# Kernel optimization log

Hardware: AMD Instinct MI355X
Metric: run time of the kernel (lower is better)

The kernel has to match this reference:

```python
import jax, jax.numpy as jnp
import numpy as np

N_NODES = 50000
N_EDGES = 1600000
F_IN = 512      # 2 * embedding_dimension
HID = 512
OUT = 4
NEG_SLOPE = 0.01  # torch LeakyReLU default


def _leaky_relu(x):
    return jnp.where(x >= 0, x, NEG_SLOPE * x)


def setup_inputs() -> dict:
    key = jax.random.key(0)
    ks = jax.random.split(key, 12)
    s_in = 1.0 / np.sqrt(F_IN)
    s_h = 1.0 / np.sqrt(HID)
    return {
        "feature": jax.random.normal(ks[0], (N_NODES, F_IN), jnp.float32),
        "edge_index": jax.random.randint(ks[1], (2, N_EDGES), 0, N_NODES, jnp.int64),
        "edge_type": jax.random.randint(ks[2], (N_EDGES,), 0, 2, jnp.int64),
        # input MLP
        "W_in": jax.random.uniform(ks[3], (F_IN, HID), jnp.float32, -s_in, s_in),
        "b_in": jnp.zeros((HID,), jnp.float32),
        # sage1: lin_l (bias) on aggregated neighbors, lin_r (no bias) on self
        "W1_l": jax.random.uniform(ks[4], (HID, HID), jnp.float32, -s_h, s_h),
        "b1_l": jnp.zeros((HID,), jnp.float32),
        "W1_r": jax.random.uniform(ks[5], (HID, HID), jnp.float32, -s_h, s_h),
        # sage2
        "W2_l": jax.random.uniform(ks[6], (HID, HID), jnp.float32, -s_h, s_h),
        "b2_l": jnp.zeros((HID,), jnp.float32),
        "W2_r": jax.random.uniform(ks[7], (HID, HID), jnp.float32, -s_h, s_h),
        # output linear (hidden -> 4); note forward skips linear_relu_output1
        "W_out": jax.random.uniform(ks[8], (HID, OUT), jnp.float32, -s_h, s_h),
        "b_out": jnp.zeros((OUT,), jnp.float32),
    }


def _sage_conv(x, src, dst, W_l, b_l, W_r):
    # mean aggregation of source features onto destinations (PyG default flow)
    agg = jax.ops.segment_sum(x[src], dst, num_segments=N_NODES)  # [N, H]
    cnt = jax.ops.segment_sum(jnp.ones((src.shape[0], 1), x.dtype), dst,
                              num_segments=N_NODES)               # [N, 1]
    mean = agg / jnp.maximum(cnt, 1.0)
    return mean @ W_l + b_l + x @ W_r


def reference(feature, edge_index, edge_type,
              W_in, b_in, W1_l, b1_l, W1_r, W2_l, b2_l, W2_r, W_out, b_out):
    src, dst = edge_index[0], edge_index[1]
    x = _leaky_relu(feature.astype(jnp.float32) @ W_in + b_in)
    x = _sage_conv(x, src, dst, W1_l, b1_l, W1_r)
    # dropout is identity in eval mode
    x = _sage_conv(x, src, dst, W2_l, b2_l, W2_r)
    return x @ W_out + b_out
```

## Files before the change

kernel.cpp:

```cpp
#include <hip/hip_runtime.h>
#include <stdint.h>

#define NNODES 50000
#define NEDGES 1600000
#define HID 512
#define NEG_SLOPE 0.01f
#define NBUCK 98
#define NBLK 200
#define TILE 8000
#define NSUB 8
#define GPBLK 391
#define MROWS 50048
#define NNB 8

#define TCBLK 1024
#define CABLK 12512
#define SABLK 1025
#define PREP_CA (TCBLK)
#define PREP_SA (TCBLK + CABLK)
#define PREP_HK (TCBLK + CABLK + SABLK)
#define PREP_GRID (PREP_HK + NBLK)

typedef __attribute__((ext_vector_type(8))) short bf16x8;
typedef __attribute__((ext_vector_type(8))) unsigned short u16x8;
typedef __attribute__((ext_vector_type(4))) float f32x4;

__device__ __forceinline__ unsigned short f2bf(float f) {
  unsigned int u = __builtin_bit_cast(unsigned int, f);
  u += 0x7FFFu + ((u >> 16) & 1u);
  return (unsigned short)(u >> 16);
}
__device__ __forceinline__ void gload_lds16(const void* g, void* l) {
  __builtin_amdgcn_global_load_lds(
      (const __attribute__((address_space(1))) void*)g,
      (__attribute__((address_space(3))) void*)l, 16, 0, 0);
}

__device__ __forceinline__ float wave_dot(const float* __restrict__ Arow,
                                          const float* __restrict__ B, int j) {
  int l = threadIdx.x & 63;
  float4 a0 = *reinterpret_cast<const float4*>(Arow + l * 8);
  float4 a1 = *reinterpret_cast<const float4*>(Arow + l * 8 + 4);
  const float* bb = B + (size_t)(l * 8) * 4 + j;
  float s = a0.x * bb[0] + a0.y * bb[4] + a0.z * bb[8] + a0.w * bb[12] +
            a1.x * bb[16] + a1.y * bb[20] + a1.z * bb[24] + a1.w * bb[28];
#pragma unroll
  for (int off = 1; off < 64; off <<= 1) s += __shfl_xor(s, off);
  return s;
}

__global__ __launch_bounds__(256) void prep(
    const float* __restrict__ feat, const float* __restrict__ W_in,
    const float* __restrict__ W2l, const float* __restrict__ W2r,
    const float* __restrict__ Wout, const float* __restrict__ b2l,
    const float* __restrict__ bout, const int* __restrict__ ei,
    unsigned short* __restrict__ Wt0, unsigned short* __restrict__ featb,
    float* __restrict__ Wlp, float* __restrict__ Wrp, float* __restrict__ bp,
    int* __restrict__ hist) {
  __shared__ int h[NBUCK];
  __shared__ int flg;
  int blk = blockIdx.x, t = threadIdx.x;
  if (blk < PREP_CA) {
    int i = blk * 256 + t;
    int n = i >> 9, k = i & 511;
    Wt0[i] = f2bf(W_in[(k << 9) | n]);
  } else if (blk < PREP_SA) {
    int idx = (blk - PREP_CA) * 256 + t;
    size_t g = (size_t)idx * 8;
    int row = idx >> 6;
    u16x8 pk;
    if (row < NNODES) {
      float4 v0 = *reinterpret_cast<const float4*>(feat + g);
      float4 v1 = *reinterpret_cast<const float4*>(feat + g + 4);
      pk[0] = f2bf(v0.x); pk[1] = f2bf(v0.y); pk[2] = f2bf(v0.z); pk[3] = f2bf(v0.w);
      pk[4] = f2bf(v1.x); pk[5] = f2bf(v1.y); pk[6] = f2bf(v1.z); pk[7] = f2bf(v1.w);
    } else {
      pk = (u16x8)0;
    }
    *reinterpret_cast<u16x8*>(featb + g) = pk;
  } else if (blk < PREP_HK) {
    int gw = (blk - PREP_SA) * 4 + (t >> 6);
    int l = t & 63;
    if (gw < 2048) {
      float v = wave_dot(W2l + (size_t)(gw >> 2) * 512, Wout, gw & 3);
      if (l == 0) Wlp[gw] = v;
    } else if (gw < 4096) {
      int g = gw - 2048;
      float v = wave_dot(W2r + (size_t)(g >> 2) * 512, Wout, g & 3);
      if (l == 0) Wrp[g] = v;
    } else if (gw < 4100) {
      int j = gw - 4096;
      float v = wave_dot(b2l, Wout, j);
      if (l == 0) bp[j] = v + bout[j];
    }
  } else {
    int hb = blk - PREP_HK;
    for (int i = t; i < NBUCK; i += 256) h[i] = 0;
    if (t < 64) {
      unsigned long long m = __ballot(ei[2 * t + 1] != 0);
      if (t == 0) flg = (m != 0ULL) ? 1 : 0;
    }
    __syncthreads();
    int f = flg;
    int e0 = hb * TILE;
    for (int e = e0 + 2 * t; e < e0 + TILE; e += 512) {
      int d0, d1;
      if (f) {
        int2 v = *reinterpret_cast<const int2*>(&ei[(size_t)NEDGES + e]);
        d0 = v.x; d1 = v.y;
      } else {
        int4 v = *reinterpret_cast<const int4*>(&ei[2 * ((size_t)NEDGES + e)]);
        d0 = v.x; d1 = v.z;
      }
      if ((unsigned)d0 < NNODES) atomicAdd(&h[d0 >> 9], 1);
      if ((unsigned)d1 < NNODES) atomicAdd(&h[d1 >> 9], 1);
    }
    __syncthreads();
    for (int i = t; i < NBUCK; i += 256) hist[i * NBLK + hb] = h[i];
  }
}

__global__ __launch_bounds__(256) void smallB(
    const float* __restrict__ W1l, const float* __restrict__ W1r,
    const float* __restrict__ b1l,
    const float* __restrict__ Wlp, const float* __restrict__ Wrp,
    const float* __restrict__ bp,
    float* __restrict__ Pall, float* __restrict__ kb, float* __restrict__ kc) {
  int gw = blockIdx.x * 4 + (threadIdx.x >> 6);
  int l = threadIdx.x & 63;
  if (gw < 6144) {
    int k = gw / 12, jg = gw % 12;
    int g = jg >> 2, j = jg & 3;
    float v;
    if (g == 0) v = wave_dot(W1l + (size_t)k * 512, Wlp, j);
    else if (g == 1) v = wave_dot(W1r + (size_t)k * 512, Wlp, j) +
                         wave_dot(W1l + (size_t)k * 512, Wrp, j);
    else v = wave_dot(W1r + (size_t)k * 512, Wrp, j);
    if (l == 0) Pall[k * 12 + jg] = v;
  } else if (gw < 6152) {
    int i = gw - 6144, j = i & 3;
    if (i < 4) {
      float v = wave_dot(b1l, Wlp, j);
      if (l == 0) kb[j] = v;
    } else {
      float v = wave_dot(b1l, Wrp, j);
      if (l == 0) kc[j] = v + bp[j];
    }
  }
}

__global__ __launch_bounds__(512) void scanh(int* __restrict__ hist,
                                             int* __restrict__ bstart) {
  __shared__ int s[512];
  const int TOT = NBUCK * NBLK;
  const int C = 40;
  int t = threadIdx.x;
  int base = t * C;
  int sum = 0;
#pragma unroll
  for (int i = 0; i < C; i++) {
    int idx = base + i;
    sum += (idx < TOT) ? hist[idx] : 0;
  }
  s[t] = sum;
  __syncthreads();
  for (int off = 1; off < 512; off <<= 1) {
    int u = (t >= off) ? s[t - off] : 0;
    __syncthreads();
    s[t] += u;
    __syncthreads();
  }
  int run = (t > 0) ? s[t - 1] : 0;
#pragma unroll
  for (int i = 0; i < C; i++) {
    int idx = base + i;
    if (idx < TOT) {
      int v = hist[idx];
      hist[idx] = run;
      if (idx % NBLK == 0) bstart[idx / NBLK] = run;
      run += v;
    }
  }
  if (t == 511) bstart[NBUCK] = s[511];
}

__global__ __launch_bounds__(256) void binscatter(const int* __restrict__ ei,
                                                  const int* __restrict__ hbase,
                                                  unsigned int* __restrict__ pcol) {
  __shared__ unsigned int vals[TILE];
  __shared__ unsigned char bid[TILE];
  __shared__ int lcnt[NBUCK];
  __shared__ int lbase[NBUCK];
  __shared__ int delta[NBUCK];
  __shared__ int flg;
  int t = threadIdx.x, blk = blockIdx.x;
  for (int i = t; i < NBUCK; i += 256) lcnt[i] = 0;
  if (t < 64) {
    unsigned long long m = __ballot(ei[2 * t + 1] != 0);
    if (t == 0) flg = (m != 0ULL) ? 1 : 0;
  }
  __syncthreads();
  int f = flg;
  int e0 = blk * TILE;
  for (int e = e0 + 2 * t; e < e0 + TILE; e += 512) {
    int d0, d1;
    if (f) {
      int2 vd = *reinterpret_cast<const int2*>(&ei[(size_t)NEDGES + e]);
      d0 = vd.x; d1 = vd.y;
    } else {
      int4 vd = *reinterpret_cast<const int4*>(&ei[2 * ((size_t)NEDGES + e)]);
      d0 = vd.x; d1 = vd.z;
    }
    if ((unsigned)d0 < NNODES) atomicAdd(&lcnt[d0 >> 9], 1);
    if ((unsigned)d1 < NNODES) atomicAdd(&lcnt[d1 >> 9], 1);
  }
  __syncthreads();
  if (t == 0) {
    int run = 0;
    for (int b = 0; b < NBUCK; b++) { lbase[b] = run; run += lcnt[b]; }
  }
  __syncthreads();
  for (int b = t; b < NBUCK; b += 256) {
    delta[b] = hbase[b * NBLK + blk] - lbase[b];
    lcnt[b] = 0;
  }
  __syncthreads();
  for (int e = e0 + 2 * t; e < e0 + TILE; e += 512) {
    int s0, s1v, d0, d1;
    if (f) {
      int2 vs = *reinterpret_cast<const int2*>(&ei[e]);
      int2 vd = *reinterpret_cast<const int2*>(&ei[(size_t)NEDGES + e]);
      s0 = vs.x; s1v = vs.y; d0 = vd.x; d1 = vd.y;
    } else {
      int4 vs = *reinterpret_cast<const int4*>(&ei[2 * (size_t)e]);
      int4 vd = *reinterpret_cast<const int4*>(&ei[2 * ((size_t)NEDGES + e)]);
      s0 = vs.x; s1v = vs.z; d0 = vd.x; d1 = vd.z;
    }
    if ((unsigned)d0 < NNODES) {
      if ((unsigned)s0 >= NNODES) s0 = 0;
      int b = d0 >> 9;
      int p = lbase[b] + atomicAdd(&lcnt[b], 1);
      vals[p] = ((unsigned)(d0 & 511) << 16) | (unsigned)s0;
      bid[p] = (unsigned char)b;
    }
    if ((unsigned)d1 < NNODES) {
      if ((unsigned)s1v >= NNODES) s1v = 0;
      int b = d1 >> 9;
      int p = lbase[b] + atomicAdd(&lcnt[b], 1);
      vals[p] = ((unsigned)(d1 & 511) << 16) | (unsigned)s1v;
      bid[p] = (unsigned char)b;
    }
  }
  __syncthreads();
  int total = lbase[NBUCK - 1] + lcnt[NBUCK - 1];
  for (int p = t; p < total; p += 256) {
    pcol[delta[bid[p]] + p] = vals[p];
  }
}

__global__ __launch_bounds__(256, 4) void gemmproj(
    const unsigned short* __restrict__ Ab, const unsigned short* __restrict__ Bt,
    const float* __restrict__ bias, const float* __restrict__ Pall,
    float* __restrict__ t0p) {
  __shared__ unsigned short As[128 * 32];
  __shared__ unsigned short Bs[64 * 32];
  __shared__ float tab[2][128 * 12];
  const int tid = threadIdx.x;
  const int wave = tid >> 6, lane = tid & 63;
  const int w = blockIdx.x;
  const int mt = (w & 7) + ((w >> 6) << 3);
  const int nb = (w >> 3) & 7;
  if (mt >= GPBLK) return;
  const int bm = mt * 128, bn = nb * 64;
  const int wr = wave >> 1, wc = wave & 1;
  const int r15 = lane & 15, kl = lane >> 4;
  const int srow = lane >> 2, soff = (lane & 3) * 8;

  for (int i = tid; i < 1536; i += 256) { tab[0][i] = 0.f; tab[1][i] = 0.f; }

  f32x4 acc[2][4];
#pragma unroll
  for (int i = 0; i < 2; i++)
#pragma unroll
    for (int j = 0; j < 4; j++) acc[i][j] = {0.f, 0.f, 0.f, 0.f};

  for (int kt = 0; kt < HID / 32; ++kt) {
#pragma unroll
    for (int rr = 0; rr < 2; ++rr) {
      int c = wave * 2 + rr;
      int row = c * 16 + srow;
      gload_lds16(Ab + (size_t)(bm + row) * HID + kt * 32 + soff, (void*)&As[c * 512]);
    }
    {
      int row = wave * 16 + srow;
      gload_lds16(Bt + (size_t)(bn + row) * HID + kt * 32 + soff, (void*)&Bs[wave * 512]);
    }
    __syncthreads();
    bf16x8 af[4], bfr[2];
#pragma unroll
    for (int mi = 0; mi < 4; ++mi)
      af[mi] = *reinterpret_cast<const bf16x8*>(&As[(wr * 64 + mi * 16 + r15) * 32 + kl * 8]);
#pragma unroll
    for (int ni = 0; ni < 2; ++ni)
      bfr[ni] = *reinterpret_cast<const bf16x8*>(&Bs[(wc * 32 + ni * 16 + r15) * 32 + kl * 8]);
#pragma unroll
    for (int ni = 0; ni < 2; ++ni)
#pragma unroll
      for (int mi = 0; mi < 4; ++mi)
        acc[ni][mi] = __builtin_amdgcn_mfma_f32_16x16x32_bf16(bfr[ni], af[mi], acc[ni][mi], 0, 0, 0);
    __syncthreads();
  }

#pragma unroll
  for (int mi = 0; mi < 4; ++mi) {
    float p12[12];
#pragma unroll
    for (int j = 0; j < 12; ++j) p12[j] = 0.f;
#pragma unroll
    for (int ni = 0; ni < 2; ++ni) {
      int nbase = bn + wc * 32 + ni * 16 + kl * 4;
      float4 bv4 = *reinterpret_cast<const float4*>(bias + nbase);
      float bb[4] = {bv4.x, bv4.y, bv4.z, bv4.w};
#pragma unroll
      for (int rg = 0; rg < 4; ++rg) {
        float v = acc[ni][mi][rg] + bb[rg];
        v = (v >= 0.f) ? v : NEG_SLOPE * v;
        const float* Pc = Pall + (size_t)(nbase + rg) * 12;
        float4 p0 = *reinterpret_cast<const float4*>(Pc);
        float4 p1 = *reinterpret_cast<const float4*>(Pc + 4);
        float4 p2 = *reinterpret_cast<const float4*>(Pc + 8);
        p12[0] += v * p0.x; p12[1] += v * p0.y; p12[2] += v * p0.z; p12[3] += v * p0.w;
        p12[4] += v * p1.x; p12[5] += v * p1.y; p12[6] += v * p1.z; p12[7] += v * p1.w;
        p12[8] += v * p2.x; p12[9] += v * p2.y; p12[10] += v * p2.z; p12[11] += v * p2.w;
      }
    }
#pragma unroll
    for (int j = 0; j < 12; ++j) {
      p12[j] += __shfl_xor(p12[j], 16);
      p12[j] += __shfl_xor(p12[j], 32);
    }
    if (kl == 0) {
      int r = wr * 64 + mi * 16 + r15;
#pragma unroll
      for (int j = 0; j < 12; ++j) tab[wc][r * 12 + j] = p12[j];
    }
  }
  __syncthreads();
  float* o = t0p + ((size_t)nb * MROWS + bm) * 12;
  for (int i = tid; i < 1536; i += 256) o[i] = tab[0][i] + tab[1][i];
}

__global__ __launch_bounds__(256) void reduce_t0(
    const float* __restrict__ t0p, float* __restrict__ t0a,
    float* __restrict__ t0b, float* __restrict__ t0c) {
  int n = blockIdx.x * 256 + threadIdx.x;
  if (n >= NNODES) return;
  float s[12];
#pragma unroll
  for (int j = 0; j < 12; ++j) s[j] = 0.f;
#pragma unroll
  for (int p = 0; p < NNB; ++p) {
    const float* q = t0p + ((size_t)p * MROWS + n) * 12;
    float4 a = *reinterpret_cast<const float4*>(q);
    float4 b = *reinterpret_cast<const float4*>(q + 4);
    float4 c = *reinterpret_cast<const float4*>(q + 8);
    s[0] += a.x; s[1] += a.y; s[2] += a.z; s[3] += a.w;
    s[4] += b.x; s[5] += b.y; s[6] += b.z; s[7] += b.w;
    s[8] += c.x; s[9] += c.y; s[10] += c.z; s[11] += c.w;
  }
  *reinterpret_cast<float4*>(t0a + (size_t)n * 4) = {s[0], s[1], s[2], s[3]};
  *reinterpret_cast<float4*>(t0b + (size_t)n * 4) = {s[4], s[5], s[6], s[7]};
  *reinterpret_cast<float4*>(t0c + (size_t)n * 4) = {s[8], s[9], s[10], s[11]};
}

__global__ __launch_bounds__(256) void aggA(
    const unsigned int* __restrict__ pcol, const int* __restrict__ bstart,
    const float* __restrict__ t0a, float* __restrict__ partialA) {
  __shared__ float tab[512 * 5];
  int t = threadIdx.x;
  int b = blockIdx.x >> 3, sb = blockIdx.x & 7;
  for (int i = t; i < 2560; i += 256) tab[i] = 0.f;
  __syncthreads();
  int st = bstart[b], en = bstart[b + 1];
  int len = en - st;
  int a0 = st + (int)(((long long)len * sb) >> 3);
  int a1 = st + (int)(((long long)len * (sb + 1)) >> 3);
  for (int e = a0 + t; e < a1; e += 256) {
    unsigned v = pcol[e];
    int i = v >> 16, src = v & 0xFFFF;
    float4 x = *reinterpret_cast<const float4*>(t0a + (size_t)src * 4);
    atomicAdd(&tab[i * 5 + 0], x.x);
    atomicAdd(&tab[i * 5 + 1], x.y);
    atomicAdd(&tab[i * 5 + 2], x.z);
    atomicAdd(&tab[i * 5 + 3], x.w);
    atomicAdd(&tab[i * 5 + 4], 1.f);
  }
  __syncthreads();
  float* o = partialA + (size_t)blockIdx.x * 2560;
  for (int i = t; i < 2560; i += 256) o[i] = tab[i];
}

__global__ __launch_bounds__(256) void finA(
    const float* __restrict__ partialA, const float* __restrict__ t0b,
    float* __restrict__ s1, float* __restrict__ degf) {
  int n = blockIdx.x * 256 + threadIdx.x;
  if (n >= NNODES) return;
  int b = n >> 9, i = n & 511;
  float a[5] = {0.f, 0.f, 0.f, 0.f, 0.f};
#pragma unroll
  for (int s = 0; s < 8; s++) {
    const float* p = partialA + (size_t)(b * 8 + s) * 2560 + i * 5;
#pragma unroll
    for (int j = 0; j < 5; j++) a[j] += p[j];
  }
  float deg = a[4];
  float sc = (deg > 0.f) ? 1.f / deg : 0.f;
  float4 tb = *reinterpret_cast<const float4*>(t0b + (size_t)n * 4);
  float4 o = {a[0] * sc + tb.x, a[1] * sc + tb.y, a[2] * sc + tb.z, a[3] * sc + tb.w};
  *reinterpret_cast<float4*>(s1 + (size_t)n * 4) = o;
  degf[n] = deg;
}

__global__ __launch_bounds__(256) void aggB(
    const unsigned int* __restrict__ pcol, const int* __restrict__ bstart,
    const float* __restrict__ s1, float* __restrict__ partialB) {
  __shared__ float tab[512 * 4];
  int t = threadIdx.x;
  int b = blockIdx.x >> 3, sb = blockIdx.x & 7;
  for (int i = t; i < 2048; i += 256) tab[i] = 0.f;
  __syncthreads();
  int st = bstart[b], en = bstart[b + 1];
  int len = en - st;
  int a0 = st + (int)(((long long)len * sb) >> 3);
  int a1 = st + (int)(((long long)len * (sb + 1)) >> 3);
  for (int e = a0 + t; e < a1; e += 256) {
    unsigned v = pcol[e];
    int i = v >> 16, src = v & 0xFFFF;
    float4 x = *reinterpret_cast<const float4*>(s1 + (size_t)src * 4);
    atomicAdd(&tab[i * 4 + 0], x.x);
    atomicAdd(&tab[i * 4 + 1], x.y);
    atomicAdd(&tab[i * 4 + 2], x.z);
    atomicAdd(&tab[i * 4 + 3], x.w);
  }
  __syncthreads();
  float* o = partialB + (size_t)blockIdx.x * 2048;
  for (int i = t; i < 2048; i += 256) o[i] = tab[i];
}

__global__ __launch_bounds__(256) void finB(
    const float* __restrict__ partialB, const float* __restrict__ t0c,
    const float* __restrict__ degf, const float* __restrict__ kb,
    const float* __restrict__ kc, float* __restrict__ out) {
  int n = blockIdx.x * 256 + threadIdx.x;
  if (n >= NNODES) return;
  int b = n >> 9, i = n & 511;
  float a[4] = {0.f, 0.f, 0.f, 0.f};
#pragma unroll
  for (int s = 0; s < 8; s++) {
    const float* p = partialB + (size_t)(b * 8 + s) * 2048 + i * 4;
#pragma unroll
    for (int j = 0; j < 4; j++) a[j] += p[j];
  }
  float deg = degf[n];
  float sc = (deg > 0.f) ? 1.f / deg : 0.f;
  float ind = (deg > 0.f) ? 1.f : 0.f;
  float4 c = *reinterpret_cast<const float4*>(t0c + (size_t)n * 4);
  float4 vb = *reinterpret_cast<const float4*>(kb);
  float4 vc = *reinterpret_cast<const float4*>(kc);
  float4 o = {a[0] * sc + c.x + ind * vb.x + vc.x,
              a[1] * sc + c.y + ind * vb.y + vc.y,
              a[2] * sc + c.z + ind * vb.z + vc.z,
              a[3] * sc + c.w + ind * vb.w + vc.w};
  *reinterpret_cast<float4*>(out + (size_t)n * 4) = o;
}

extern "C" void kernel_launch(void* const* d_in, const int* in_sizes, int n_in,
                              void* d_out, int out_size, void* d_ws, size_t ws_size,
                              hipStream_t stream) {
  const float* feat = (const float*)d_in[0];
  const int* ei = (const int*)d_in[1];
  const float* W_in = (const float*)d_in[3];
  const float* b_in = (const float*)d_in[4];
  const float* W1l = (const float*)d_in[5];
  const float* b1l = (const float*)d_in[6];
  const float* W1r = (const float*)d_in[7];
  const float* W2l = (const float*)d_in[8];
  const float* b2l = (const float*)d_in[9];
  const float* W2r = (const float*)d_in[10];
  const float* Wout = (const float*)d_in[11];
  const float* bout = (const float*)d_in[12];
  float* out = (float*)d_out;

  char* ws = (char*)d_ws;
  size_t off = 0;
  auto alloc = [&](size_t bytes) {
    void* p = ws + off;
    off += (bytes + 15) & ~(size_t)15;
    return p;
  };
  float* t0a  = (float*)alloc((size_t)MROWS * 4 * 4);
  float* t0b  = (float*)alloc((size_t)MROWS * 4 * 4);
  float* t0c  = (float*)alloc((size_t)MROWS * 4 * 4);
  float* partialA = (float*)alloc((size_t)NBUCK * NSUB * 2560 * 4);
  float* partialB = (float*)alloc((size_t)NBUCK * NSUB * 2048 * 4);
  float* t0p  = (float*)alloc((size_t)NNB * MROWS * 12 * 4);
  int* hist   = (int*)alloc((size_t)NBUCK * NBLK * 4);
  int* bstart = (int*)alloc((NBUCK + 1) * 4);
  unsigned int* pcol = (unsigned int*)alloc((size_t)NEDGES * 4);
  unsigned short* featb = (unsigned short*)alloc((size_t)MROWS * HID * 2);
  unsigned short* Wt0 = (unsigned short*)alloc(512 * 512 * 2);
  float* Wlp  = (float*)alloc(2048 * 4);
  float* Wrp  = (float*)alloc(2048 * 4);
  float* bp   = (float*)alloc(16);
  float* Pall = (float*)alloc(512 * 12 * 4);
  float* kb   = (float*)alloc(16);
  float* kc   = (float*)alloc(16);
  float* s1   = (float*)alloc((size_t)MROWS * 4 * 4);
  float* degf = (float*)alloc((size_t)NNODES * 4);
  (void)ws_size;

  prep<<<PREP_GRID, 256, 0, stream>>>(feat, W_in, W2l, W2r, Wout, b2l, bout, ei,
                                      Wt0, featb, Wlp, Wrp, bp, hist);
  smallB<<<1538, 256, 0, stream>>>(W1l, W1r, b1l, Wlp, Wrp, bp, Pall, kb, kc);

  scanh<<<1, 512, 0, stream>>>(hist, bstart);
  binscatter<<<NBLK, 256, 0, stream>>>(ei, hist, pcol);

  gemmproj<<<49 * 64, 256, 0, stream>>>(featb, Wt0, b_in, Pall, t0p);
  reduce_t0<<<(NNODES + 255) / 256, 256, 0, stream>>>(t0p, t0a, t0b, t0c);
  aggA<<<NBUCK * NSUB, 256, 0, stream>>>(pcol, bstart, t0a, partialA);
  finA<<<(NNODES + 255) / 256, 256, 0, stream>>>(partialA, t0b, s1, degf);
  aggB<<<NBUCK * NSUB, 256, 0, stream>>>(pcol, bstart, s1, partialB);
  finB<<<(NNODES + 255) / 256, 256, 0, stream>>>(partialB, t0c, degf, kb, kc, out);
}
```

Measured before the change: 301.2 us.

## Software-pipeline gemmproj global-to-LDS loads with a four-slot ring buffer

Replaces the single-buffered A/B LDS tiles in the projection GEMM with a four-slot shared-memory ring. Loads run two k-steps ahead, and explicit vmcnt waits plus raw barriers replace the per-iteration __syncthreads pairs. The aim is to overlap global-memory latency with the MFMA work instead of stalling on every k-tile. The epilogue reduction table now reuses the same shared buffer, and the unneeded zero-init of the table is dropped. In exchange, LDS use per block rises to 48 KB and the occupancy hint drops from 4 to 3 blocks per CU.

```diff
diff --git a/kernel.cpp b/kernel.cpp
--- a/kernel.cpp
+++ b/kernel.cpp
@@ -258,13 +258,11 @@
   }
 }
 
-__global__ __launch_bounds__(256, 4) void gemmproj(
+__global__ __launch_bounds__(256, 3) void gemmproj(
     const unsigned short* __restrict__ Ab, const unsigned short* __restrict__ Bt,
     const float* __restrict__ bias, const float* __restrict__ Pall,
     float* __restrict__ t0p) {
-  __shared__ unsigned short As[128 * 32];
-  __shared__ unsigned short Bs[64 * 32];
-  __shared__ float tab[2][128 * 12];
+  __shared__ __align__(16) char smem[49152];
   const int tid = threadIdx.x;
   const int wave = tid >> 6, lane = tid & 63;
   const int w = blockIdx.x;
@@ -275,8 +273,10 @@
   const int wr = wave >> 1, wc = wave & 1;
   const int r15 = lane & 15, kl = lane >> 4;
   const int srow = lane >> 2, soff = (lane & 3) * 8;
-
-  for (int i = tid; i < 1536; i += 256) { tab[0][i] = 0.f; tab[1][i] = 0.f; }
+  const int c0 = wave * 2, c1 = wave * 2 + 1;
+  const unsigned short* gA0 = Ab + (size_t)(bm + c0 * 16 + srow) * HID + soff;
+  const unsigned short* gA1 = Ab + (size_t)(bm + c1 * 16 + srow) * HID + soff;
+  const unsigned short* gB0 = Bt + (size_t)(bn + wave * 16 + srow) * HID + soff;
 
   f32x4 acc[2][4];
 #pragma unroll
@@ -284,32 +284,47 @@
 #pragma unroll
     for (int j = 0; j < 4; j++) acc[i][j] = {0.f, 0.f, 0.f, 0.f};
 
-  for (int kt = 0; kt < HID / 32; ++kt) {
-#pragma unroll
-    for (int rr = 0; rr < 2; ++rr) {
-      int c = wave * 2 + rr;
-      int row = c * 16 + srow;
-      gload_lds16(Ab + (size_t)(bm + row) * HID + kt * 32 + soff, (void*)&As[c * 512]);
-    }
-    {
-      int row = wave * 16 + srow;
-      gload_lds16(Bt + (size_t)(bn + row) * HID + kt * 32 + soff, (void*)&Bs[wave * 512]);
-    }
-    __syncthreads();
+#define STAGE(j)                                                              \
+  do {                                                                        \
+    unsigned short* as_ = (unsigned short*)(smem + ((j) & 3) * 12288);        \
+    unsigned short* bs_ = (unsigned short*)(smem + ((j) & 3) * 12288 + 8192); \
+    const int ko_ = (j) * 32;                                                 \
+    gload_lds16(gA0 + ko_, (void*)&as_[c0 * 512]);                            \
+    gload_lds16(gA1 + ko_, (void*)&as_[c1 * 512]);                            \
+    gload_lds16(gB0 + ko_, (void*)&bs_[wave * 512]);                          \
+  } while (0)
+
+  STAGE(0);
+  STAGE(1);
+
+#pragma unroll
+  for (int kt = 0; kt < 16; ++kt) {
+    if (kt + 2 < 16) STAGE(kt + 2);
+    if (kt < 14)      asm volatile("s_waitcnt vmcnt(6)" ::: "memory");
+    else if (kt == 14) asm volatile("s_waitcnt vmcnt(3)" ::: "memory");
+    else               asm volatile("s_waitcnt vmcnt(0)" ::: "memory");
+    __builtin_amdgcn_s_barrier();
+    const unsigned short* as_ = (const unsigned short*)(smem + (kt & 3) * 12288);
+    const unsigned short* bs_ = (const unsigned short*)(smem + (kt & 3) * 12288 + 8192);
     bf16x8 af[4], bfr[2];
 #pragma unroll
     for (int mi = 0; mi < 4; ++mi)
-      af[mi] = *reinterpret_cast<const bf16x8*>(&As[(wr * 64 + mi * 16 + r15) * 32 + kl * 8]);
+      af[mi] = *reinterpret_cast<const bf16x8*>(&as_[(wr * 64 + mi * 16 + r15) * 32 + kl * 8]);
 #pragma unroll
     for (int ni = 0; ni < 2; ++ni)
-      bfr[ni] = *reinterpret_cast<const bf16x8*>(&Bs[(wc * 32 + ni * 16 + r15) * 32 + kl * 8]);
+      bfr[ni] = *reinterpret_cast<const bf16x8*>(&bs_[(wc * 32 + ni * 16 + r15) * 32 + kl * 8]);
 #pragma unroll
     for (int ni = 0; ni < 2; ++ni)
 #pragma unroll
       for (int mi = 0; mi < 4; ++mi)
         acc[ni][mi] = __builtin_amdgcn_mfma_f32_16x16x32_bf16(bfr[ni], af[mi], acc[ni][mi], 0, 0, 0);
-    __syncthreads();
-  }
+    __builtin_amdgcn_s_barrier();
+  }
+#undef STAGE
+
+  __syncthreads();
+  float* tab0 = (float*)smem;
+  float* tab1 = (float*)(smem + 6144);
 
 #pragma unroll
   for (int mi = 0; mi < 4; ++mi) {
@@ -341,13 +356,14 @@
     }
     if (kl == 0) {
       int r = wr * 64 + mi * 16 + r15;
-#pragma unroll
-      for (int j = 0; j < 12; ++j) tab[wc][r * 12 + j] = p12[j];
+      float* tb = wc ? tab1 : tab0;
+#pragma unroll
+      for (int j = 0; j < 12; ++j) tb[r * 12 + j] = p12[j];
     }
   }
   __syncthreads();
   float* o = t0p + ((size_t)nb * MROWS + bm) * 12;
-  for (int i = tid; i < 1536; i += 256) o[i] = tab[0][i] + tab[1][i];
+  for (int i = tid; i < 1536; i += 256) o[i] = tab0[i] + tab1[i];
 }
 
 __global__ __launch_bounds__(256) void reduce_t0(
```

After: 295.0 us. 2.0% less time.
